# Kernel tuning notes

Measured on AMD Instinct MI355X. Metric: run time of the kernel, lower is better.

Reference implementation:

```python
import jax, jax.numpy as jnp
import numpy as np

EMBED_DIM = 1024
NUM_HEADS = 16
HEAD_DIM = EMBED_DIM // NUM_HEADS


def setup_inputs() -> dict:
    key = jax.random.key(0)
    k_x, k_qw, k_qb, k_ow, k_ob = jax.random.split(key, 5)
    B, T, C = 4, 2048, EMBED_DIM
    s = 1.0 / np.sqrt(C)
    return {
        "x": jax.random.normal(k_x, (B, T, C), dtype=jnp.float32),
        # torch nn.Linear weights: [out_features, in_features]
        "qkv_w": jax.random.uniform(k_qw, (3 * C, C), jnp.float32, -s, s),
        "qkv_b": jax.random.uniform(k_qb, (3 * C,), jnp.float32, -s, s),
        "out_w": jax.random.uniform(k_ow, (C, C), jnp.float32, -s, s),
        "out_b": jax.random.uniform(k_ob, (C,), jnp.float32, -s, s),
    }


def reference(x, qkv_w, qkv_b, out_w, out_b):
    B, T, C = x.shape
    H, D = NUM_HEADS, HEAD_DIM
    qkv = x @ qkv_w.T + qkv_b                      # [B,T,3C]
    qkv = qkv.reshape(B, T, 3, H, D).transpose(2, 0, 3, 1, 4)  # [3,B,H,T,D]
    Q, K, V = qkv[0], qkv[1], qkv[2]
    scores = jnp.einsum("bhtd,bhsd->bhts", Q, K) / np.sqrt(D).astype(np.float32)
    causal = jnp.triu(jnp.ones((T, T), dtype=bool), k=1)        # mask future
    scores = jnp.where(causal, -jnp.inf, scores)
    attn_weights = jax.nn.softmax(scores, axis=-1)              # [B,H,T,T]
    out = jnp.einsum("bhts,bhsd->bhtd", attn_weights, V)
    out = out.transpose(0, 2, 1, 3).reshape(B, T, C)
    return out @ out_w.T + out_b, attn_weights
```

## Files before the change

kernel.cpp:

```cpp
#include <hip/hip_runtime.h>
#include <cstdint>
#include <cstddef>

#define Bq  4
#define Tq  2048
#define Cq  1024
#define Hq  16
#define Dq  64
#define BTq 8192
#define C3q 3072

using bf16x8 = __attribute__((ext_vector_type(8))) short;
using f32x4  = __attribute__((ext_vector_type(4))) float;
using us4    = __attribute__((ext_vector_type(4))) unsigned short;

__device__ __forceinline__ unsigned short f2bf(float f) {
  unsigned u = __builtin_bit_cast(unsigned, f);
  return (unsigned short)((u + 0x7fffu + ((u >> 16) & 1u)) >> 16);
}
__device__ __forceinline__ float bf2f(unsigned short h) {
  return __builtin_bit_cast(float, (unsigned)h << 16);
}

__device__ __forceinline__ void gload_lds16(const void* g, void* l) {
  __builtin_amdgcn_global_load_lds(
      (const __attribute__((address_space(1))) void*)g,
      (__attribute__((address_space(3))) void*)l, 16, 0, 0);
}

__global__ __launch_bounds__(256) void cvt_kernel(const float* __restrict__ src,
                                                  unsigned short* __restrict__ dst, int n4) {
  int i = blockIdx.x * 256 + threadIdx.x;
  int stride = gridDim.x * 256;
  for (; i < n4; i += stride) {
    float4 v = reinterpret_cast<const float4*>(src)[i];
    us4 o = { f2bf(v.x), f2bf(v.y), f2bf(v.z), f2bf(v.w) };
    reinterpret_cast<us4*>(dst)[i] = o;
  }
}

template<int EPI>
__global__ __launch_bounds__(256) void gemm128(
    const unsigned short* __restrict__ A, const unsigned short* __restrict__ Bw,
    const float* __restrict__ bias,
    unsigned short* __restrict__ Qb, unsigned short* __restrict__ Kb,
    unsigned short* __restrict__ Vtb, float* __restrict__ Cout,
    int M, int N, int K)
{
  __shared__ __align__(16) unsigned short S[8704];
  unsigned short* As = S;
  unsigned short* Bs = S + 4096;
  const int n0 = blockIdx.x * 128, m0 = blockIdx.y * 128;
  const int tid = threadIdx.x;
  const int w = tid >> 6, l = tid & 63, r = l & 15, g = l >> 4;
  const int wm = w >> 1, wn = w & 1;
  const int ldRow = tid >> 2, ldCol = (tid & 3) * 8;
  f32x4 acc[4][4] = {};

  const unsigned short* Ar0 = A  + (size_t)(m0 +      ldRow) * K + ldCol;
  const unsigned short* Ar1 = A  + (size_t)(m0 + 64 + ldRow) * K + ldCol;
  const unsigned short* Br0 = Bw + (size_t)(n0 +      ldRow) * K + ldCol;
  const unsigned short* Br1 = Bw + (size_t)(n0 + 64 + ldRow) * K + ldCol;
  char* Ab0 = (char*)As        + w * 1024;
  char* Ab1 = (char*)As + 4096 + w * 1024;
  char* Bb0 = (char*)Bs        + w * 1024;
  char* Bb1 = (char*)Bs + 4096 + w * 1024;

  for (int k0 = 0; k0 < K; k0 += 32) {
    __syncthreads();
    gload_lds16(Ar0 + k0, Ab0);
    gload_lds16(Ar1 + k0, Ab1);
    gload_lds16(Br0 + k0, Bb0);
    gload_lds16(Br1 + k0, Bb1);
    __syncthreads();
    bf16x8 a[4], b[4];
    #pragma unroll
    for (int i = 0; i < 4; ++i) a[i] = *(const bf16x8*)&As[(wm*64 + i*16 + r)*32 + g*8];
    #pragma unroll
    for (int j = 0; j < 4; ++j) b[j] = *(const bf16x8*)&Bs[(wn*64 + j*16 + r)*32 + g*8];
    #pragma unroll
    for (int i = 0; i < 4; ++i)
      #pragma unroll
      for (int j = 0; j < 4; ++j)
        acc[i][j] = __builtin_amdgcn_mfma_f32_16x16x32_bf16(a[i], b[j], acc[i][j], 0, 0, 0);
  }

  if (EPI == 0) {
    const int which = n0 >> 10;
    __syncthreads();
    #pragma unroll
    for (int hh = 0; hh < 2; ++hh) {
      if (hh) __syncthreads();
      if (wn == hh) {
        #pragma unroll
        for (int i = 0; i < 4; ++i)
          #pragma unroll
          for (int j = 0; j < 4; ++j) {
            int c = j*16 + r;
            float bv = bias[n0 + hh*64 + c];
            int t = wm*64 + i*16 + 4*g;
            us4 pk = { f2bf(acc[i][j][0]+bv), f2bf(acc[i][j][1]+bv),
                       f2bf(acc[i][j][2]+bv), f2bf(acc[i][j][3]+bv) };
            *(us4*)&S[c*136 + t] = pk;
          }
      }
      __syncthreads();
      const int hd = (n0 & 1023) + hh*64;
      const int h  = hd >> 6;
      if (which == 2) {
        int d = tid >> 2, tp = tid & 3;
        int bh = (m0 >> 11)*Hq + h;
        size_t base = ((size_t)(bh*Dq + d))*Tq + (m0 & 2047) + tp*32;
        const unsigned short* Lr = &S[d*136 + tp*32];
        #pragma unroll
        for (int q4 = 0; q4 < 4; ++q4)
          *(bf16x8*)&Vtb[base + q4*8] = *(const bf16x8*)&Lr[q4*8];
      } else {
        unsigned short* dst = which ? Kb : Qb;
        int t = tid >> 1, dp = tid & 1;
        int gr = m0 + t;
        int bh = (gr >> 11)*Hq + h;
        size_t base = ((size_t)(bh*Tq + (gr & 2047)))*Dq + dp*32;
        #pragma unroll
        for (int q4 = 0; q4 < 4; ++q4) {
          bf16x8 vv;
          #pragma unroll
          for (int e = 0; e < 8; ++e)
            vv[e] = (short)S[(dp*32 + q4*8 + e)*136 + t];
          *(bf16x8*)&dst[base + q4*8] = vv;
        }
      }
    }
  } else {
    #pragma unroll
    for (int i = 0; i < 4; ++i)
      #pragma unroll
      for (int j = 0; j < 4; ++j) {
        int gc = n0 + wn*64 + j*16 + r;
        float bv = bias[gc];
        #pragma unroll
        for (int jj = 0; jj < 4; ++jj) {
          int gr = m0 + wm*64 + i*16 + 4*g + jj;
          Cout[(size_t)gr * N + gc] = acc[i][j][jj] + bv;
        }
      }
  }
}

#define PROWB 4224
#define XMASK(row_) ((((row_) & 7) << 4) ^ ((((row_) >> 2) & 3) << 5))

__global__ __launch_bounds__(512, 4) void attn_kernel(
    const unsigned short* __restrict__ Qb, const unsigned short* __restrict__ Kb,
    const unsigned short* __restrict__ Vtb,
    float* __restrict__ attn, unsigned short* __restrict__ ctxb)
{
  __shared__ __align__(16) unsigned short P[16][2112];
  __shared__ float red[8][32];
  __shared__ float invl_s[32];

  const int p  = blockIdx.x;
  const int bh = blockIdx.y;
  const int tid = threadIdx.x, w = tid >> 6, l = tid & 63, r = l & 15, g = l >> 4;
  const int qbA = p * 16, qbB = (127 - p) * 16;
  const int NA = (qbA + 16 + 31) >> 5;
  const int NB = (qbB + 16 + 31) >> 5;
  const int LAc = NA * 32, LBc = NB * 32;
  const int nzA = 64 - NA;

  const unsigned short* Qp = Qb  + (size_t)bh * Tq * Dq;
  const unsigned short* Kp = Kb  + (size_t)bh * Tq * Dq;
  const unsigned short* Vp = Vtb + (size_t)bh * Dq * Tq;
  char* Pmut = (char*)&P[0][0];

  bf16x8 aqA0 = *(const bf16x8*)&Qp[(size_t)(qbA + r)*Dq      + g*8];
  bf16x8 aqA1 = *(const bf16x8*)&Qp[(size_t)(qbA + r)*Dq + 32 + g*8];
  bf16x8 aqB0 = *(const bf16x8*)&Qp[(size_t)(qbB + r)*Dq      + g*8];
  bf16x8 aqB1 = *(const bf16x8*)&Qp[(size_t)(qbB + r)*Dq + 32 + g*8];

  float lsumA[4] = {0.f,0.f,0.f,0.f}, lsumB[4] = {0.f,0.f,0.f,0.f};

#define LOADK(ci_, D00, D01, D10, D11)                                              \
  {                                                                                 \
    int cj_ = ((ci_) < NA) ? (ci_) : (ci_) - NA;                                    \
    int k0c_ = cj_ * 32;                                                            \
    D00 = *(const bf16x8*)&Kp[(size_t)(k0c_ + r)*Dq      + g*8];                    \
    D01 = *(const bf16x8*)&Kp[(size_t)(k0c_ + r)*Dq + 32 + g*8];                    \
    D10 = *(const bf16x8*)&Kp[(size_t)(k0c_ + 16 + r)*Dq      + g*8];               \
    D11 = *(const bf16x8*)&Kp[(size_t)(k0c_ + 16 + r)*Dq + 32 + g*8];               \
  }

  {
    const f32x4 zero4 = {0.f,0.f,0.f,0.f};
    bf16x8 k00, k01, k10, k11, n00, n01, n10, n11;
    int ci = w;
    if (ci < 65) LOADK(ci, k00, k01, k10, k11);
    for (; ci < 65; ci += 8) {
      if (ci + 8 < 65) LOADK(ci + 8, n00, n01, n10, n11);
      if (ci < 63) {
        int zq, zc;
        if (ci < nzA) { zq = qbA; zc = LAc + ci*32; }
        else          { zq = qbB; zc = LBc + (ci - nzA)*32; }
        size_t zb = ((size_t)bh*Tq + zq + (l >> 2))*Tq + zc + (l & 3)*8;
        __builtin_nontemporal_store(zero4, (f32x4*)&attn[zb]);
        __builtin_nontemporal_store(zero4, (f32x4*)&attn[zb + 4]);
      }
      const bool isA = ci < NA;
      const int cj  = isA ? ci : ci - NA;
      const int k0c = cj * 32;
      const int qb_ = isA ? qbA : qbB;
      const int cb_ = isA ? k0c : LAc + k0c;
      bf16x8 q0_ = isA ? aqA0 : aqB0;
      bf16x8 q1_ = isA ? aqA1 : aqB1;
      f32x4 z = {0.f,0.f,0.f,0.f};
      __builtin_amdgcn_s_setprio(1);
      f32x4 s0 = __builtin_amdgcn_mfma_f32_16x16x32_bf16(q0_, k00, z, 0, 0, 0);
      s0 = __builtin_amdgcn_mfma_f32_16x16x32_bf16(q1_, k01, s0, 0, 0, 0);
      f32x4 s1 = __builtin_amdgcn_mfma_f32_16x16x32_bf16(q0_, k10, z, 0, 0, 0);
      s1 = __builtin_amdgcn_mfma_f32_16x16x32_bf16(q1_, k11, s1, 0, 0, 0);
      __builtin_amdgcn_s_setprio(0);
      float tch[4];
      #pragma unroll
      for (int jj = 0; jj < 4; ++jj) {
        int q = qb_ + 4*g + jj;
        float p0 = (k0c + r      <= q) ? __expf(s0[jj]*0.125f) : 0.f;
        float p1 = (k0c + 16 + r <= q) ? __expf(s1[jj]*0.125f) : 0.f;
        tch[jj] = p0 + p1;
        int row = 4*g + jj, xm = XMASK(row);
        *(unsigned short*)(Pmut + row*PROWB + (((cb_ + r)*2)      ^ xm)) = f2bf(p0);
        *(unsigned short*)(Pmut + row*PROWB + (((cb_ + 16 + r)*2) ^ xm)) = f2bf(p1);
      }
      if (isA) { lsumA[0]+=tch[0]; lsumA[1]+=tch[1]; lsumA[2]+=tch[2]; lsumA[3]+=tch[3]; }
      else     { lsumB[0]+=tch[0]; lsumB[1]+=tch[1]; lsumB[2]+=tch[2]; lsumB[3]+=tch[3]; }
      k00 = n00; k01 = n01; k10 = n10; k11 = n11;
    }
  }

  #pragma unroll
  for (int jj = 0; jj < 4; ++jj) {
    float sa = lsumA[jj], sb = lsumB[jj];
    #pragma unroll
    for (int off = 1; off < 16; off <<= 1) {
      sa += __shfl_xor(sa, off, 64);
      sb += __shfl_xor(sb, off, 64);
    }
    if (r == 0) { red[w][4*g + jj] = sa; red[w][16 + 4*g + jj] = sb; }
  }
  __syncthreads();
  if (tid < 32) {
    float s = 0.f;
    #pragma unroll
    for (int ww = 0; ww < 8; ++ww) s += red[ww][tid];
    invl_s[tid] = 1.f / s;
  }
  __syncthreads();

  if (w < 4) {
    #pragma unroll
    for (int s = 0; s < 2; ++s) {
      const int idx   = s * 256 + tid;
      const int s16   = idx >> 8;
      const int row16 = (idx >> 4) & 15;
      const int seg   = (idx & 15) * 8;
      const int xm16  = XMASK(row16);
      const char* Prow = Pmut + row16 * PROWB;
      const int Lc    = s16 ? LBc : LAc;
      const int cbase = s16 ? LAc : 0;
      float inv = invl_s[s16*16 + row16];
      size_t ob = ((size_t)bh*Tq + (s16 ? qbB : qbA) + row16) * Tq;
      for (int cb = seg; cb < Lc; cb += 128) {
        bf16x8 pv = *(const bf16x8*)(Prow + (((cbase + cb)*2) ^ xm16));
        f32x4 v0, v1;
        v0[0]=bf2f((unsigned short)pv[0])*inv; v0[1]=bf2f((unsigned short)pv[1])*inv;
        v0[2]=bf2f((unsigned short)pv[2])*inv; v0[3]=bf2f((unsigned short)pv[3])*inv;
        v1[0]=bf2f((unsigned short)pv[4])*inv; v1[1]=bf2f((unsigned short)pv[5])*inv;
        v1[2]=bf2f((unsigned short)pv[6])*inv; v1[3]=bf2f((unsigned short)pv[7])*inv;
        __builtin_nontemporal_store(v0, (f32x4*)&attn[ob + cb]);
        __builtin_nontemporal_store(v1, (f32x4*)&attn[ob + cb + 4]);
      }
    }
  } else {
    const int dblk = w - 4;
    const char* Pr = Pmut + r * PROWB;
    const int xr = XMASK(r);
    const unsigned short* Vrow = &Vp[(size_t)(dblk*16 + r) * Tq];
    f32x4 coA0 = {0.f,0.f,0.f,0.f}, coA1 = {0.f,0.f,0.f,0.f};
    f32x4 coB0 = {0.f,0.f,0.f,0.f}, coB1 = {0.f,0.f,0.f,0.f};
    bf16x8 pa, bv, pan, bvn;
    {
      pa = *(const bf16x8*)(Pr + (((0 + g*8)*2) ^ xr));
      bv = *(const bf16x8*)&Vrow[g*8];
    }
    for (int ci = 0; ci < 65; ++ci) {
      if (ci + 1 < 65) {
        int cn = ci + 1;
        int cj = (cn < NA) ? cn : cn - NA;
        int cb = (cn < NA) ? cn*32 : LAc + cj*32;
        pan = *(const bf16x8*)(Pr + (((cb + g*8)*2) ^ xr));
        bvn = *(const bf16x8*)&Vrow[cj*32 + g*8];
      }
      if (ci < NA) {
        if (ci & 1) coA1 = __builtin_amdgcn_mfma_f32_16x16x32_bf16(pa, bv, coA1, 0, 0, 0);
        else        coA0 = __builtin_amdgcn_mfma_f32_16x16x32_bf16(pa, bv, coA0, 0, 0, 0);
      } else {
        if (ci & 1) coB1 = __builtin_amdgcn_mfma_f32_16x16x32_bf16(pa, bv, coB1, 0, 0, 0);
        else        coB0 = __builtin_amdgcn_mfma_f32_16x16x32_bf16(pa, bv, coB0, 0, 0, 0);
      }
      pa = pan; bv = bvn;
    }
    const int b = bh >> 4, h = bh & 15;
    #pragma unroll
    for (int jj = 0; jj < 4; ++jj) {
      int tA = qbA + 4*g + jj;
      ctxb[(size_t)(b*Tq + tA)*Cq + h*Dq + dblk*16 + r] =
          f2bf((coA0[jj] + coA1[jj]) * invl_s[4*g + jj]);
      int tB = qbB + 4*g + jj;
      ctxb[(size_t)(b*Tq + tB)*Cq + h*Dq + dblk*16 + r] =
          f2bf((coB0[jj] + coB1[jj]) * invl_s[16 + 4*g + jj]);
    }
  }
#undef LOADK
}

extern "C" void kernel_launch(void* const* d_in, const int* in_sizes, int n_in,
                              void* d_out, int out_size, void* d_ws, size_t ws_size,
                              hipStream_t stream) {
  const float* x     = (const float*)d_in[0];
  const float* qkv_w = (const float*)d_in[1];
  const float* qkv_b = (const float*)d_in[2];
  const float* out_w = (const float*)d_in[3];
  const float* out_b = (const float*)d_in[4];
  float* out  = (float*)d_out;
  float* attn = out + (size_t)BTq * Cq;

  char* ws = (char*)d_ws;
  unsigned short* xb    = (unsigned short*)(ws);
  unsigned short* wqkvb = (unsigned short*)(ws + (16u << 20));
  unsigned short* woutb = (unsigned short*)(ws + (22u << 20));
  unsigned short* Qb    = (unsigned short*)(ws + (24u << 20));
  unsigned short* Kb    = (unsigned short*)(ws + (40u << 20));
  unsigned short* Vtb   = (unsigned short*)(ws + (56u << 20));
  unsigned short* ctxb  = (unsigned short*)(ws + (72u << 20));

  cvt_kernel<<<2048, 256, 0, stream>>>(x,     xb,    (BTq * Cq) / 4);
  cvt_kernel<<<1024, 256, 0, stream>>>(qkv_w, wqkvb, (C3q * Cq) / 4);
  cvt_kernel<<<512,  256, 0, stream>>>(out_w, woutb, (Cq * Cq) / 4);

  dim3 g1(C3q / 128, BTq / 128);
  gemm128<0><<<g1, 256, 0, stream>>>(xb, wqkvb, qkv_b, Qb, Kb, Vtb, nullptr, BTq, C3q, Cq);

  dim3 g2(64, Bq * Hq);
  attn_kernel<<<g2, 512, 0, stream>>>(Qb, Kb, Vtb, attn, ctxb);

  dim3 g3(Cq / 128, BTq / 128);
  gemm128<1><<<g3, 256, 0, stream>>>(ctxb, woutb, out_b, nullptr, nullptr, nullptr, out, BTq, Cq, Cq);
}
```

Baseline: 493.1 us.

## Pack two 8-row query tiles into one MFMA tile and halve attention block size

The attention kernel now gives each 256-thread block 8 rows from the front and 8 rows from the back of the sequence. Both halves are packed into a single 16-row MFMA operand, so each K chunk is multiplied once instead of once per half. The grid doubles to 128 blocks per head. Zero-fill of the masked region is moved to a per-row strided loop, and the PV stage pulls V straight from global memory without prefetch. This removes redundant QK MFMAs, but work is wasted on masked-out chunks for the short rows, and the V loads lose their software pipelining.

New measurement: 590.1 us. 19.7% more time.

```diff
diff --git a/kernel.cpp b/kernel.cpp
--- a/kernel.cpp
+++ b/kernel.cpp
@@ -147,176 +147,160 @@
   }
 }
 
-#define PROWB 4224
-#define XMASK(row_) ((((row_) & 7) << 4) ^ ((((row_) >> 2) & 3) << 5))
-
-__global__ __launch_bounds__(512, 4) void attn_kernel(
+#define XM(ir_) (((ir_) & 7) << 4)
+
+__global__ __launch_bounds__(256, 4) void attn_kernel(
     const unsigned short* __restrict__ Qb, const unsigned short* __restrict__ Kb,
     const unsigned short* __restrict__ Vtb,
     float* __restrict__ attn, unsigned short* __restrict__ ctxb)
 {
-  __shared__ __align__(16) unsigned short P[16][2112];
-  __shared__ float red[8][32];
-  __shared__ float invl_s[32];
+  __shared__ __align__(16) char Pm[35456];
+  __shared__ float red[4][16];
+  __shared__ float invl_s[16];
 
   const int p  = blockIdx.x;
   const int bh = blockIdx.y;
   const int tid = threadIdx.x, w = tid >> 6, l = tid & 63, r = l & 15, g = l >> 4;
-  const int qbA = p * 16, qbB = (127 - p) * 16;
-  const int NA = (qbA + 16 + 31) >> 5;
-  const int NB = (qbB + 16 + 31) >> 5;
-  const int LAc = NA * 32, LBc = NB * 32;
-  const int nzA = 64 - NA;
+  const int qbA = p * 8, qbB = 2040 - p * 8;
+  const int NAc = (8*p + 39) >> 5;
+  const int NBc = 65 - NAc;
+  const int LA = NAc * 32, LB = NBc * 32;
+  const int RAb = (LA*2 + 127) & ~127;
+  const int RBb = (LB*2 + 127) & ~127;
 
   const unsigned short* Qp = Qb  + (size_t)bh * Tq * Dq;
   const unsigned short* Kp = Kb  + (size_t)bh * Tq * Dq;
   const unsigned short* Vp = Vtb + (size_t)bh * Dq * Tq;
-  char* Pmut = (char*)&P[0][0];
-
-  bf16x8 aqA0 = *(const bf16x8*)&Qp[(size_t)(qbA + r)*Dq      + g*8];
-  bf16x8 aqA1 = *(const bf16x8*)&Qp[(size_t)(qbA + r)*Dq + 32 + g*8];
-  bf16x8 aqB0 = *(const bf16x8*)&Qp[(size_t)(qbB + r)*Dq      + g*8];
-  bf16x8 aqB1 = *(const bf16x8*)&Qp[(size_t)(qbB + r)*Dq + 32 + g*8];
-
-  float lsumA[4] = {0.f,0.f,0.f,0.f}, lsumB[4] = {0.f,0.f,0.f,0.f};
-
-#define LOADK(ci_, D00, D01, D10, D11)                                              \
+
+  const int qrow = (r < 8) ? (qbA + r) : (qbB + r - 8);
+  bf16x8 aq0 = *(const bf16x8*)&Qp[(size_t)qrow*Dq      + g*8];
+  bf16x8 aq1 = *(const bf16x8*)&Qp[(size_t)qrow*Dq + 32 + g*8];
+
+  int qe[4], rb[4];
+  #pragma unroll
+  for (int jj = 0; jj < 4; ++jj) {
+    int ir = 4*g + jj;
+    qe[jj] = (ir < 8) ? (qbA + ir) : (qbB + ir - 8);
+    rb[jj] = (ir < 8) ? ir*RAb : 8*RAb + (ir-8)*RBb;
+  }
+  const bool isArow = (g < 2);
+
+  const int irz   = tid >> 4;
+  const int Lrow  = (irz < 8) ? LA : LB;
+  const int qgz   = (irz < 8) ? (qbA + irz) : (qbB + irz - 8);
+  int zcol        = Lrow + (tid & 15) * 8;
+  float* zrow = &attn[((size_t)bh*Tq + qgz) * Tq];
+  const f32x4 zero4 = {0.f,0.f,0.f,0.f};
+
+  float lsum[4] = {0.f,0.f,0.f,0.f};
+
+#define LOADK(k0_, D00, D01, D10, D11)                                              \
   {                                                                                 \
-    int cj_ = ((ci_) < NA) ? (ci_) : (ci_) - NA;                                    \
-    int k0c_ = cj_ * 32;                                                            \
-    D00 = *(const bf16x8*)&Kp[(size_t)(k0c_ + r)*Dq      + g*8];                    \
-    D01 = *(const bf16x8*)&Kp[(size_t)(k0c_ + r)*Dq + 32 + g*8];                    \
-    D10 = *(const bf16x8*)&Kp[(size_t)(k0c_ + 16 + r)*Dq      + g*8];               \
-    D11 = *(const bf16x8*)&Kp[(size_t)(k0c_ + 16 + r)*Dq + 32 + g*8];               \
+    D00 = *(const bf16x8*)&Kp[(size_t)((k0_) + r)*Dq      + g*8];                   \
+    D01 = *(const bf16x8*)&Kp[(size_t)((k0_) + r)*Dq + 32 + g*8];                   \
+    D10 = *(const bf16x8*)&Kp[(size_t)((k0_) + 16 + r)*Dq      + g*8];              \
+    D11 = *(const bf16x8*)&Kp[(size_t)((k0_) + 16 + r)*Dq + 32 + g*8];              \
   }
 
   {
-    const f32x4 zero4 = {0.f,0.f,0.f,0.f};
     bf16x8 k00, k01, k10, k11, n00, n01, n10, n11;
     int ci = w;
-    if (ci < 65) LOADK(ci, k00, k01, k10, k11);
-    for (; ci < 65; ci += 8) {
-      if (ci + 8 < 65) LOADK(ci + 8, n00, n01, n10, n11);
-      if (ci < 63) {
-        int zq, zc;
-        if (ci < nzA) { zq = qbA; zc = LAc + ci*32; }
-        else          { zq = qbB; zc = LBc + (ci - nzA)*32; }
-        size_t zb = ((size_t)bh*Tq + zq + (l >> 2))*Tq + zc + (l & 3)*8;
-        __builtin_nontemporal_store(zero4, (f32x4*)&attn[zb]);
-        __builtin_nontemporal_store(zero4, (f32x4*)&attn[zb + 4]);
-      }
-      const bool isA = ci < NA;
-      const int cj  = isA ? ci : ci - NA;
-      const int k0c = cj * 32;
-      const int qb_ = isA ? qbA : qbB;
-      const int cb_ = isA ? k0c : LAc + k0c;
-      bf16x8 q0_ = isA ? aqA0 : aqB0;
-      bf16x8 q1_ = isA ? aqA1 : aqB1;
+    if (ci < NBc) LOADK(ci*32, k00, k01, k10, k11);
+    for (; ci < NBc; ci += 4) {
+      if (ci + 4 < NBc) LOADK((ci+4)*32, n00, n01, n10, n11);
+      #pragma unroll
+      for (int zu = 0; zu < 2; ++zu)
+        if (zcol < Tq) {
+          __builtin_nontemporal_store(zero4, (f32x4*)&zrow[zcol]);
+          __builtin_nontemporal_store(zero4, (f32x4*)&zrow[zcol + 4]);
+          zcol += 128;
+        }
+      const int k0c = ci * 32;
       f32x4 z = {0.f,0.f,0.f,0.f};
       __builtin_amdgcn_s_setprio(1);
-      f32x4 s0 = __builtin_amdgcn_mfma_f32_16x16x32_bf16(q0_, k00, z, 0, 0, 0);
-      s0 = __builtin_amdgcn_mfma_f32_16x16x32_bf16(q1_, k01, s0, 0, 0, 0);
-      f32x4 s1 = __builtin_amdgcn_mfma_f32_16x16x32_bf16(q0_, k10, z, 0, 0, 0);
-      s1 = __builtin_amdgcn_mfma_f32_16x16x32_bf16(q1_, k11, s1, 0, 0, 0);
+      f32x4 s0 = __builtin_amdgcn_mfma_f32_16x16x32_bf16(aq0, k00, z, 0, 0, 0);
+      s0 = __builtin_amdgcn_mfma_f32_16x16x32_bf16(aq1, k01, s0, 0, 0, 0);
+      f32x4 s1 = __builtin_amdgcn_mfma_f32_16x16x32_bf16(aq0, k10, z, 0, 0, 0);
+      s1 = __builtin_amdgcn_mfma_f32_16x16x32_bf16(aq1, k11, s1, 0, 0, 0);
       __builtin_amdgcn_s_setprio(0);
-      float tch[4];
+      const bool wrA = !isArow || (k0c < LA);
+      const int j0 = k0c + r, j1 = k0c + 16 + r;
       #pragma unroll
       for (int jj = 0; jj < 4; ++jj) {
-        int q = qb_ + 4*g + jj;
-        float p0 = (k0c + r      <= q) ? __expf(s0[jj]*0.125f) : 0.f;
-        float p1 = (k0c + 16 + r <= q) ? __expf(s1[jj]*0.125f) : 0.f;
-        tch[jj] = p0 + p1;
-        int row = 4*g + jj, xm = XMASK(row);
-        *(unsigned short*)(Pmut + row*PROWB + (((cb_ + r)*2)      ^ xm)) = f2bf(p0);
-        *(unsigned short*)(Pmut + row*PROWB + (((cb_ + 16 + r)*2) ^ xm)) = f2bf(p1);
+        float p0 = (j0 <= qe[jj]) ? __expf(s0[jj]*0.125f) : 0.f;
+        float p1 = (j1 <= qe[jj]) ? __expf(s1[jj]*0.125f) : 0.f;
+        lsum[jj] += p0 + p1;
+        if (wrA) {
+          int ir = 4*g + jj, xm = XM(ir);
+          *(unsigned short*)(Pm + rb[jj] + ((j0*2) ^ xm)) = f2bf(p0);
+          *(unsigned short*)(Pm + rb[jj] + ((j1*2) ^ xm)) = f2bf(p1);
+        }
       }
-      if (isA) { lsumA[0]+=tch[0]; lsumA[1]+=tch[1]; lsumA[2]+=tch[2]; lsumA[3]+=tch[3]; }
-      else     { lsumB[0]+=tch[0]; lsumB[1]+=tch[1]; lsumB[2]+=tch[2]; lsumB[3]+=tch[3]; }
       k00 = n00; k01 = n01; k10 = n10; k11 = n11;
+    }
+    for (; zcol < Tq; zcol += 128) {
+      __builtin_nontemporal_store(zero4, (f32x4*)&zrow[zcol]);
+      __builtin_nontemporal_store(zero4, (f32x4*)&zrow[zcol + 4]);
     }
   }
 
   #pragma unroll
   for (int jj = 0; jj < 4; ++jj) {
-    float sa = lsumA[jj], sb = lsumB[jj];
-    #pragma unroll
-    for (int off = 1; off < 16; off <<= 1) {
-      sa += __shfl_xor(sa, off, 64);
-      sb += __shfl_xor(sb, off, 64);
-    }
-    if (r == 0) { red[w][4*g + jj] = sa; red[w][16 + 4*g + jj] = sb; }
+    float s = lsum[jj];
+    s += __shfl_xor(s, 1, 64); s += __shfl_xor(s, 2, 64);
+    s += __shfl_xor(s, 4, 64); s += __shfl_xor(s, 8, 64);
+    if (r == 0) red[w][4*g + jj] = s;
   }
   __syncthreads();
-  if (tid < 32) {
-    float s = 0.f;
-    #pragma unroll
-    for (int ww = 0; ww < 8; ++ww) s += red[ww][tid];
+  if (tid < 16) {
+    float s = red[0][tid] + red[1][tid] + red[2][tid] + red[3][tid];
     invl_s[tid] = 1.f / s;
   }
   __syncthreads();
 
-  if (w < 4) {
-    #pragma unroll
-    for (int s = 0; s < 2; ++s) {
-      const int idx   = s * 256 + tid;
-      const int s16   = idx >> 8;
-      const int row16 = (idx >> 4) & 15;
-      const int seg   = (idx & 15) * 8;
-      const int xm16  = XMASK(row16);
-      const char* Prow = Pmut + row16 * PROWB;
-      const int Lc    = s16 ? LBc : LAc;
-      const int cbase = s16 ? LAc : 0;
-      float inv = invl_s[s16*16 + row16];
-      size_t ob = ((size_t)bh*Tq + (s16 ? qbB : qbA) + row16) * Tq;
-      for (int cb = seg; cb < Lc; cb += 128) {
-        bf16x8 pv = *(const bf16x8*)(Prow + (((cbase + cb)*2) ^ xm16));
-        f32x4 v0, v1;
-        v0[0]=bf2f((unsigned short)pv[0])*inv; v0[1]=bf2f((unsigned short)pv[1])*inv;
-        v0[2]=bf2f((unsigned short)pv[2])*inv; v0[3]=bf2f((unsigned short)pv[3])*inv;
-        v1[0]=bf2f((unsigned short)pv[4])*inv; v1[1]=bf2f((unsigned short)pv[5])*inv;
-        v1[2]=bf2f((unsigned short)pv[6])*inv; v1[3]=bf2f((unsigned short)pv[7])*inv;
-        __builtin_nontemporal_store(v0, (f32x4*)&attn[ob + cb]);
-        __builtin_nontemporal_store(v1, (f32x4*)&attn[ob + cb + 4]);
-      }
+  if (w < 2) {
+    const int ir = tid >> 3, k = tid & 7;
+    const int Lr = (ir < 8) ? LA : LB;
+    const int rbase = (ir < 8) ? ir*RAb : 8*RAb + (ir-8)*RBb;
+    const int xm = XM(ir);
+    const int qg = (ir < 8) ? (qbA + ir) : (qbB + ir - 8);
+    const float inv = invl_s[ir];
+    float* orow = &attn[((size_t)bh*Tq + qg) * Tq];
+    for (int c = k*8; c < Lr; c += 64) {
+      bf16x8 pv = *(const bf16x8*)(Pm + rbase + ((c*2) ^ xm));
+      f32x4 v0, v1;
+      v0[0]=bf2f((unsigned short)pv[0])*inv; v0[1]=bf2f((unsigned short)pv[1])*inv;
+      v0[2]=bf2f((unsigned short)pv[2])*inv; v0[3]=bf2f((unsigned short)pv[3])*inv;
+      v1[0]=bf2f((unsigned short)pv[4])*inv; v1[1]=bf2f((unsigned short)pv[5])*inv;
+      v1[2]=bf2f((unsigned short)pv[6])*inv; v1[3]=bf2f((unsigned short)pv[7])*inv;
+      __builtin_nontemporal_store(v0, (f32x4*)&orow[c]);
+      __builtin_nontemporal_store(v1, (f32x4*)&orow[c + 4]);
     }
   } else {
-    const int dblk = w - 4;
-    const char* Pr = Pmut + r * PROWB;
-    const int xr = XMASK(r);
-    const unsigned short* Vrow = &Vp[(size_t)(dblk*16 + r) * Tq];
-    f32x4 coA0 = {0.f,0.f,0.f,0.f}, coA1 = {0.f,0.f,0.f,0.f};
-    f32x4 coB0 = {0.f,0.f,0.f,0.f}, coB1 = {0.f,0.f,0.f,0.f};
-    bf16x8 pa, bv, pan, bvn;
-    {
-      pa = *(const bf16x8*)(Pr + (((0 + g*8)*2) ^ xr));
-      bv = *(const bf16x8*)&Vrow[g*8];
-    }
-    for (int ci = 0; ci < 65; ++ci) {
-      if (ci + 1 < 65) {
-        int cn = ci + 1;
-        int cj = (cn < NA) ? cn : cn - NA;
-        int cb = (cn < NA) ? cn*32 : LAc + cj*32;
-        pan = *(const bf16x8*)(Pr + (((cb + g*8)*2) ^ xr));
-        bvn = *(const bf16x8*)&Vrow[cj*32 + g*8];
-      }
-      if (ci < NA) {
-        if (ci & 1) coA1 = __builtin_amdgcn_mfma_f32_16x16x32_bf16(pa, bv, coA1, 0, 0, 0);
-        else        coA0 = __builtin_amdgcn_mfma_f32_16x16x32_bf16(pa, bv, coA0, 0, 0, 0);
-      } else {
-        if (ci & 1) coB1 = __builtin_amdgcn_mfma_f32_16x16x32_bf16(pa, bv, coB1, 0, 0, 0);
-        else        coB0 = __builtin_amdgcn_mfma_f32_16x16x32_bf16(pa, bv, coB0, 0, 0, 0);
-      }
-      pa = pan; bv = bvn;
+    const int d0 = (w - 2) * 2;
+    const int prbase = (r < 8) ? r*RAb : 8*RAb + (r-8)*RBb;
+    const int xr = XM(r);
+    const unsigned short* Vr0 = &Vp[(size_t)((d0  )*16 + r) * Tq];
+    const unsigned short* Vr1 = &Vp[(size_t)((d0+1)*16 + r) * Tq];
+    f32x4 co0 = {0.f,0.f,0.f,0.f}, co1 = {0.f,0.f,0.f,0.f};
+    for (int ci = 0; ci < NBc; ++ci) {
+      const int k0c = ci * 32;
+      bf16x8 pa = *(const bf16x8*)(Pm + prbase + (((k0c + g*8)*2) ^ xr));
+      if (r < 8 && k0c >= LA) pa = bf16x8{0,0,0,0,0,0,0,0};
+      bf16x8 bv0 = *(const bf16x8*)&Vr0[k0c + g*8];
+      bf16x8 bv1 = *(const bf16x8*)&Vr1[k0c + g*8];
+      co0 = __builtin_amdgcn_mfma_f32_16x16x32_bf16(pa, bv0, co0, 0, 0, 0);
+      co1 = __builtin_amdgcn_mfma_f32_16x16x32_bf16(pa, bv1, co1, 0, 0, 0);
     }
     const int b = bh >> 4, h = bh & 15;
     #pragma unroll
     for (int jj = 0; jj < 4; ++jj) {
-      int tA = qbA + 4*g + jj;
-      ctxb[(size_t)(b*Tq + tA)*Cq + h*Dq + dblk*16 + r] =
-          f2bf((coA0[jj] + coA1[jj]) * invl_s[4*g + jj]);
-      int tB = qbB + 4*g + jj;
-      ctxb[(size_t)(b*Tq + tB)*Cq + h*Dq + dblk*16 + r] =
-          f2bf((coB0[jj] + coB1[jj]) * invl_s[16 + 4*g + jj]);
+      int ir = 4*g + jj;
+      int t = (ir < 8) ? (qbA + ir) : (qbB + ir - 8);
+      float inv = invl_s[ir];
+      size_t base = (size_t)(b*Tq + t)*Cq + h*Dq + r;
+      ctxb[base + (d0  )*16] = f2bf(co0[jj] * inv);
+      ctxb[base + (d0+1)*16] = f2bf(co1[jj] * inv);
     }
   }
 #undef LOADK
@@ -349,8 +333,8 @@
   dim3 g1(C3q / 128, BTq / 128);
   gemm128<0><<<g1, 256, 0, stream>>>(xb, wqkvb, qkv_b, Qb, Kb, Vtb, nullptr, BTq, C3q, Cq);
 
-  dim3 g2(64, Bq * Hq);
-  attn_kernel<<<g2, 512, 0, stream>>>(Qb, Kb, Vtb, attn, ctxb);
+  dim3 g2(128, Bq * Hq);
+  attn_kernel<<<g2, 256, 0, stream>>>(Qb, Kb, Vtb, attn, ctxb);
 
   dim3 g3(Cq / 128, BTq / 128);
   gemm128<1><<<g3, 256, 0, stream>>>(ctxb, woutb, out_b, nullptr, nullptr, nullptr, out, BTq, Cq, Cq);
```

## Move causal-zero attention stores from attention kernel into QKV GEMM main loop

Applied to the files above, without the earlier changes.

Writes the zero region of the attention-weight matrix (the masked future positions) from inside the QKV projection GEMM's K-loop instead of from the attention kernel. The GEMM is compute-bound, so the memory-bound zero stores can overlap its MFMA work and the attention kernel no longer carries them. The cost is extra store traffic and index arithmetic inside the GEMM loop, which could slow the GEMM. Correctness depends on the precise per-row coverage mapping matching the attention kernel's written columns.

Result: slower. 516.0 us (+4.6%).

```diff
diff --git a/kernel.cpp b/kernel.cpp
--- a/kernel.cpp
+++ b/kernel.cpp
@@ -45,6 +45,7 @@
     const float* __restrict__ bias,
     unsigned short* __restrict__ Qb, unsigned short* __restrict__ Kb,
     unsigned short* __restrict__ Vtb, float* __restrict__ Cout,
+    float* __restrict__ attnZ,
     int M, int N, int K)
 {
   __shared__ __align__(16) unsigned short S[8704];
@@ -66,6 +67,10 @@
   char* Bb0 = (char*)Bs        + w * 1024;
   char* Bb1 = (char*)Bs + 4096 + w * 1024;
 
+  const int zbase = (blockIdx.y * gridDim.x + blockIdx.x) * 43;
+  int zu = 0;
+  const f32x4 zero4 = {0.f,0.f,0.f,0.f};
+
   for (int k0 = 0; k0 < K; k0 += 32) {
     __syncthreads();
     gload_lds16(Ar0 + k0, Ab0);
@@ -73,6 +78,25 @@
     gload_lds16(Br0 + k0, Bb0);
     gload_lds16(Br1 + k0, Bb1);
     __syncthreads();
+    if (EPI == 0) {
+      #pragma unroll
+      for (int zi = 0; zi < 3; ++zi, ++zu) {
+        if (zu < 86) {
+          int pu = zbase + (zu >> 1);
+          if (pu < 65536) {
+            int zbh = pu >> 10, zp = pu & 1023;
+            int q = (zu & 1) ? (2047 - zp) : zp;
+            int Lc = ((((q >> 4) << 4) + 47) >> 5) << 5;
+            int c = Lc + tid * 8;
+            if (c < Tq) {
+              size_t zb = ((size_t)zbh * Tq + q) * Tq + c;
+              __builtin_nontemporal_store(zero4, (f32x4*)&attnZ[zb]);
+              __builtin_nontemporal_store(zero4, (f32x4*)&attnZ[zb + 4]);
+            }
+          }
+        }
+      }
+    }
     bf16x8 a[4], b[4];
     #pragma unroll
     for (int i = 0; i < 4; ++i) a[i] = *(const bf16x8*)&As[(wm*64 + i*16 + r)*32 + g*8];
@@ -166,7 +190,6 @@
   const int NA = (qbA + 16 + 31) >> 5;
   const int NB = (qbB + 16 + 31) >> 5;
   const int LAc = NA * 32, LBc = NB * 32;
-  const int nzA = 64 - NA;
 
   const unsigned short* Qp = Qb  + (size_t)bh * Tq * Dq;
   const unsigned short* Kp = Kb  + (size_t)bh * Tq * Dq;
@@ -191,20 +214,11 @@
   }
 
   {
-    const f32x4 zero4 = {0.f,0.f,0.f,0.f};
     bf16x8 k00, k01, k10, k11, n00, n01, n10, n11;
     int ci = w;
     if (ci < 65) LOADK(ci, k00, k01, k10, k11);
     for (; ci < 65; ci += 8) {
       if (ci + 8 < 65) LOADK(ci + 8, n00, n01, n10, n11);
-      if (ci < 63) {
-        int zq, zc;
-        if (ci < nzA) { zq = qbA; zc = LAc + ci*32; }
-        else          { zq = qbB; zc = LBc + (ci - nzA)*32; }
-        size_t zb = ((size_t)bh*Tq + zq + (l >> 2))*Tq + zc + (l & 3)*8;
-        __builtin_nontemporal_store(zero4, (f32x4*)&attn[zb]);
-        __builtin_nontemporal_store(zero4, (f32x4*)&attn[zb + 4]);
-      }
       const bool isA = ci < NA;
       const int cj  = isA ? ci : ci - NA;
       const int k0c = cj * 32;
@@ -347,11 +361,13 @@
   cvt_kernel<<<512,  256, 0, stream>>>(out_w, woutb, (Cq * Cq) / 4);
 
   dim3 g1(C3q / 128, BTq / 128);
-  gemm128<0><<<g1, 256, 0, stream>>>(xb, wqkvb, qkv_b, Qb, Kb, Vtb, nullptr, BTq, C3q, Cq);
+  gemm128<0><<<g1, 256, 0, stream>>>(xb, wqkvb, qkv_b, Qb, Kb, Vtb, nullptr, attn,
+                                     BTq, C3q, Cq);
 
   dim3 g2(64, Bq * Hq);
   attn_kernel<<<g2, 512, 0, stream>>>(Qb, Kb, Vtb, attn, ctxb);
 
   dim3 g3(Cq / 128, BTq / 128);
-  gemm128<1><<<g3, 256, 0, stream>>>(ctxb, woutb, out_b, nullptr, nullptr, nullptr, out, BTq, Cq, Cq);
-}
+  gemm128<1><<<g3, 256, 0, stream>>>(ctxb, woutb, out_b, nullptr, nullptr, nullptr,
+                                     out, nullptr, BTq, Cq, Cq);
+}
```
